# Kernel tuning notes

Hardware: AMD Instinct MI355X
Metric: run time of the kernel (lower is better)

## Reference

```python
import jax, jax.numpy as jnp
import numpy as np

B, C, H, W = 128, 512, 14, 14
WIN, SHIFT = 7, 3
HEADS, HD = 16, 32
HID = 2048
EPS = 1e-5
N = WIN * WIN
NWH = H // WIN
NW = NWH * NWH


def _rel_pos_index():
    coords = np.stack(np.meshgrid(np.arange(WIN), np.arange(WIN), indexing='ij'))  # (2,Wh,Ww)
    flat = coords.reshape(2, -1)
    rel = (flat[:, :, None] - flat[:, None, :]).transpose(1, 2, 0)  # (N,N,2)
    rel[..., 0] += WIN - 1
    rel[..., 1] += WIN - 1
    rel[..., 0] *= 2 * WIN - 1
    return rel.sum(-1)  # (N,N) in [0, (2W-1)^2)


def _attn_mask():
    img = np.zeros((H, W))
    cnt = 0
    for h in (slice(0, -WIN), slice(-WIN, -SHIFT), slice(-SHIFT, None)):
        for w in (slice(0, -WIN), slice(-WIN, -SHIFT), slice(-SHIFT, None)):
            img[h, w] = cnt
            cnt += 1
    mw = img.reshape(NWH, WIN, NWH, WIN).transpose(0, 2, 1, 3).reshape(-1, N)  # (nW,N)
    d = mw[:, None, :] - mw[:, :, None]
    return np.where(d != 0, -100.0, 0.0).astype(np.float32)  # (nW,N,N)


REL_IDX = _rel_pos_index()
ATTN_MASK = jnp.asarray(_attn_mask())


def _ln_c(x, w, b):
    # LayerNorm2d: normalize over channel dim of NCHW
    mu = x.mean(axis=1, keepdims=True)
    var = ((x - mu) ** 2).mean(axis=1, keepdims=True)
    xn = (x - mu) * jax.lax.rsqrt(var + EPS)
    return xn * w[None, :, None, None] + b[None, :, None, None]


def setup_inputs() -> dict:
    key = jax.random.key(0)
    ks = jax.random.split(key, 12)
    s = 0.02
    return {
        'x': jax.random.normal(ks[0], (B, C, H, W), jnp.float32),
        'ln1_w': jnp.ones((C,), jnp.float32),
        'ln1_b': jnp.zeros((C,), jnp.float32),
        'qkv_w': jax.random.normal(ks[1], (3 * C, C), jnp.float32) * s,
        'qkv_b': jnp.zeros((3 * C,), jnp.float32),
        'rel_bias': jax.random.normal(ks[2], ((2 * WIN - 1) ** 2, HEADS), jnp.float32) * s,
        'proj_w': jax.random.normal(ks[3], (C, C), jnp.float32) * s,
        'proj_b': jnp.zeros((C,), jnp.float32),
        'gamma1': jnp.full((C,), 1e-6, jnp.float32),
        'ln2_w': jnp.ones((C,), jnp.float32),
        'ln2_b': jnp.zeros((C,), jnp.float32),
        'fc1_w': jax.random.normal(ks[4], (HID, C), jnp.float32) * s,
        'fc1_b': jnp.zeros((HID,), jnp.float32),
        'fc2_w': jax.random.normal(ks[5], (C, HID), jnp.float32) * s,
        'fc2_b': jnp.zeros((C,), jnp.float32),
        'gamma2': jnp.full((C,), 1e-6, jnp.float32),
    }


def reference(x, ln1_w, ln1_b, qkv_w, qkv_b, rel_bias, proj_w, proj_b, gamma1,
              ln2_w, ln2_b, fc1_w, fc1_b, fc2_w, fc2_b, gamma2):
    # ---- shifted-window attention branch ----
    y = _ln_c(x, ln1_w, ln1_b).transpose(0, 2, 3, 1)  # (B,H,W,C)
    y = jnp.roll(y, (-SHIFT, -SHIFT), axis=(1, 2))
    # window partition -> (B*nW, N, C)
    xw = y.reshape(B, NWH, WIN, NWH, WIN, C).transpose(0, 1, 3, 2, 4, 5).reshape(B * NW, N, C)
    qkv = (xw @ qkv_w.T + qkv_b).reshape(B * NW, N, 3, HEADS, HD).transpose(2, 0, 3, 1, 4)
    q, k, v = qkv[0], qkv[1], qkv[2]  # (B*nW, heads, N, hd)
    attn = jnp.einsum('bhnd,bhmd->bhnm', q * (HD ** -0.5), k)
    bias = rel_bias[REL_IDX.reshape(-1)].reshape(N, N, HEADS).transpose(2, 0, 1)  # (heads,N,N)
    attn = attn + bias[None]
    attn = attn.reshape(B, NW, HEADS, N, N) + ATTN_MASK[None, :, None]
    attn = jax.nn.softmax(attn.reshape(B * NW, HEADS, N, N), axis=-1)
    out = jnp.einsum('bhnm,bhmd->bhnd', attn, v).transpose(0, 2, 1, 3).reshape(B * NW, N, C)
    out = out @ proj_w.T + proj_b
    # window reverse + roll back
    y = out.reshape(B, NWH, NWH, WIN, WIN, C).transpose(0, 1, 3, 2, 4, 5).reshape(B, H, W, C)
    y = jnp.roll(y, (SHIFT, SHIFT), axis=(1, 2))
    y = gamma1 * y  # layer scale over channel (last dim in NHWC)
    x = x + y.transpose(0, 3, 1, 2)
    # ---- MLP branch ----
    z = _ln_c(x, ln2_w, ln2_b).transpose(0, 2, 3, 1)  # (B,H,W,C)
    z = jax.nn.gelu(z @ fc1_w.T + fc1_b, approximate=False)
    z = z @ fc2_w.T + fc2_b
    z = gamma2 * z
    return x + z.transpose(0, 3, 1, 2)
```

## Files before the change

kernel.cpp:

```cpp
#include <hip/hip_runtime.h>
#include <cmath>
#include <cstdint>

typedef float floatx4 __attribute__((ext_vector_type(4)));

#define EPS_ 1e-5f
#define QSCALE 0.17677669529663689f

__device__ __forceinline__ void gload16(const uint8_t* g, uint8_t* l) {
  __builtin_amdgcn_global_load_lds(
      (const __attribute__((address_space(1))) void*)g,
      (__attribute__((address_space(3))) void*)l, 16, 0, 0);
}

template<bool HI>
__device__ __forceinline__ int pk_fp8(float a, float b, int old) {
  return __builtin_amdgcn_cvt_pk_fp8_f32(a, b, old, HI);
}
__device__ __forceinline__ int pk_fp8x4(float v0, float v1, float v2, float v3) {
  int w = pk_fp8<false>(v0, v1, 0);
  return pk_fp8<true>(v2, v3, w);
}

__device__ __forceinline__ uint16_t f2bf(float f) {
  uint32_t u = __float_as_uint(f);
  return (uint16_t)((u + 0x7fffu + ((u >> 16) & 1u)) >> 16);
}
__device__ __forceinline__ float bf2f(uint16_t h) {
  return __uint_as_float(((uint32_t)h) << 16);
}

__device__ __forceinline__ float fast_gelu(float v) {
  const float t = __expf(-1.702f * v);
  return v * __builtin_amdgcn_rcpf(1.f + t);
}


template<int K>
__global__ void cvt_frag(const float* __restrict__ s, uint8_t* __restrict__ d, int n4) {
  const int i = blockIdx.x * 256 + threadIdx.x;
  if (i >= n4) return;
  const int kq = K >> 2;
  const int n = i / kq;
  const int k = (i - n * kq) << 2;
  const float4 v = ((const float4*)s)[i];
  const int panel = ((n >> 6) << 2) + (n & 3);
  const int lm = (n >> 2) & 15;
  const long addr = (long)panel * (16 * K) + ((k >> 3) << 7) + (lm << 3) + (k & 4);
  *(int*)(d + addr) = pk_fp8x4(v.x, v.y, v.z, v.w);
}

__global__ __launch_bounds__(256)
void ln_stats_nchw(const float* __restrict__ x, float* __restrict__ mu, float* __restrict__ rs) {
  const int tl = threadIdx.x & 63;
  const int wv = threadIdx.x >> 6;
  const int t = blockIdx.x * 64 + tl;
  const int b = t / 196;
  const int p = t - b * 196;
  const float* xp = x + (long)b * 100352 + p;
  float s = 0.f, ss = 0.f;
  const int cbeg = wv * 128;
  for (int c = cbeg; c < cbeg + 128; ++c) {
    const float v = xp[(long)c * 196];
    s += v; ss += v * v;
  }
  __shared__ float sb[4][64], qb[4][64];
  sb[wv][tl] = s; qb[wv][tl] = ss;
  __syncthreads();
  if (wv == 0) {
    s  = sb[0][tl] + sb[1][tl] + sb[2][tl] + sb[3][tl];
    ss = qb[0][tl] + qb[1][tl] + qb[2][tl] + qb[3][tl];
    const float m = s * (1.f / 512.f);
    const float var = ss * (1.f / 512.f) - m * m;
    mu[t] = m;
    rs[t] = rsqrtf(var + EPS_);
  }
}

__global__ __launch_bounds__(256)
void ln1_apply(const float* __restrict__ x, const float* __restrict__ mu, const float* __restrict__ rs,
               const float* __restrict__ w, const float* __restrict__ bb, uint8_t* __restrict__ A) {
  __shared__ float tile[64][53];
  const int bid = blockIdx.x;
  const int ct = bid & 7;
  const int pt = (bid >> 3) & 3;
  const int b = bid >> 5;
  const int p0 = pt * 49, c0 = ct * 64;
  const long xbase = (long)b * 100352;
  for (int idx = threadIdx.x; idx < 3136; idx += 256) {
    const int cl = idx / 49;
    const int pl = idx - cl * 49;
    tile[cl][pl] = x[xbase + (long)(c0 + cl) * 196 + p0 + pl];
  }
  __syncthreads();
  const int tbase = b * 196 + p0;
  for (int idx = threadIdx.x; idx < 784; idx += 256) {
    const int pl = idx >> 4;
    const int cq = (idx & 15) << 2;
    const int t = tbase + pl;
    const int c = c0 + cq;
    const float m = mu[t], rr = rs[t];
    const float v0 = (tile[cq + 0][pl] - m) * rr * w[c + 0] + bb[c + 0];
    const float v1 = (tile[cq + 1][pl] - m) * rr * w[c + 1] + bb[c + 1];
    const float v2 = (tile[cq + 2][pl] - m) * rr * w[c + 2] + bb[c + 2];
    const float v3 = (tile[cq + 3][pl] - m) * rr * w[c + 3] + bb[c + 3];
    const long addr = (long)(t & ~15) * 512 + ((c >> 3) << 7) + ((t & 15) << 3) + (c & 4);
    *(int*)(A + addr) = pk_fp8x4(v0, v1, v2, v3);
  }
}

__global__ __launch_bounds__(256)
void ln2_panel(const uint16_t* __restrict__ Xb, const float* __restrict__ S1,
               const float* __restrict__ S2, const float* __restrict__ w,
               const float* __restrict__ bb, uint8_t* __restrict__ Z) {
  __shared__ float xs[16 * 516];
  const int p = blockIdx.x;
  const int t0 = p * 16;
  for (int idx = threadIdx.x; idx < 1024; idx += 256) {
    const int tl = idx >> 6;
    const int c8 = (idx & 63) << 3;
    const uint4 raw = *(const uint4*)(Xb + ((long)(t0 + tl) << 9) + c8);
    float* xr = xs + tl * 516 + c8;
    xr[0] = bf2f((uint16_t)(raw.x & 0xffff)); xr[1] = bf2f((uint16_t)(raw.x >> 16));
    xr[2] = bf2f((uint16_t)(raw.y & 0xffff)); xr[3] = bf2f((uint16_t)(raw.y >> 16));
    xr[4] = bf2f((uint16_t)(raw.z & 0xffff)); xr[5] = bf2f((uint16_t)(raw.z >> 16));
    xr[6] = bf2f((uint16_t)(raw.w & 0xffff)); xr[7] = bf2f((uint16_t)(raw.w >> 16));
  }
  __syncthreads();
  uint8_t* zp = Z + (long)p * 8192;
  for (int e = threadIdx.x; e < 2048; e += 256) {
    const int off = e << 2;
    const int k8 = off >> 7;
    const int tl = (off >> 3) & 15;
    const int c = (k8 << 3) + (off & 4);
    const int t = t0 + tl;
    const float m = S1[t] * (1.f / 512.f);
    const float var = S2[t] * (1.f / 512.f) - m * m;
    const float r = rsqrtf(var + EPS_);
    const float* xr = xs + tl * 516 + c;
    const float v0 = (xr[0] - m) * r * w[c + 0] + bb[c + 0];
    const float v1 = (xr[1] - m) * r * w[c + 1] + bb[c + 1];
    const float v2 = (xr[2] - m) * r * w[c + 2] + bb[c + 2];
    const float v3 = (xr[3] - m) * r * w[c + 3] + bb[c + 3];
    *(int*)(zp + off) = pk_fp8x4(v0, v1, v2, v3);
  }
}

template<int MI, int K, int EPI, int NG, int T>
__global__ __launch_bounds__(256, 4)
void gemm_bl(const uint8_t* __restrict__ A, const uint8_t* __restrict__ Bw,
             const float* __restrict__ bias, const float* __restrict__ res,
             const uint16_t* __restrict__ resb, const float* __restrict__ gamma,
             uint8_t* __restrict__ outb, float* __restrict__ outf,
             uint16_t* __restrict__ outh, float* __restrict__ S1, float* __restrict__ S2,
             const int N) {
  const int kx = blockIdx.x & 7;
  const int sx = blockIdx.x >> 3;
  const int t = (sx / NG) * 8 + kx;
  if (t >= T) return;
  const int g = sx - (sx / NG) * NG;
  __shared__ __align__(16) uint8_t Bs[(EPI == 3) ? 33280 : 32768];
  const int tid = threadIdx.x;
  const int wave = tid >> 6, lane = tid & 63;
  const int lm = lane & 15, lq = lane >> 4;
  const long m0 = (long)t * (MI * 64);
  const long n0 = (long)g << 6;
  const uint8_t* abase = A + (m0 + wave * MI * 16) * (long)K + (lane << 3);
  floatx4 acc[MI][4] = {};
  constexpr int NKS = K / 32;
  long aP0[MI], aP1[MI];
  #pragma unroll
  for (int i = 0; i < MI; ++i) {
    aP0[i] = *(const long*)(abase + (long)i * 16 * K);
    aP1[i] = *(const long*)(abase + (long)i * 16 * K + 512);
  }
  #pragma unroll
  for (int ph = 0; ph < K / 512; ++ph) {
    const uint8_t* bsrc = Bw + n0 * K + ph * 8192;
    #pragma unroll
    for (int j = 0; j < 4; ++j)
      #pragma unroll
      for (int c = 0; c < 2; ++c)
        gload16(bsrc + (long)j * 16 * K + c * 4096 + tid * 16,
                Bs + j * 8192 + c * 4096 + tid * 16);
    __syncthreads();
    #pragma unroll
    for (int ksl = 0; ksl < 16; ++ksl) {
      const int sg = ph * 16 + ksl;
      long aC[MI];
      #pragma unroll
      for (int i = 0; i < MI; ++i) aC[i] = (ksl & 1) ? aP1[i] : aP0[i];
      if (sg + 2 < NKS) {
        #pragma unroll
        for (int i = 0; i < MI; ++i) {
          const long v = *(const long*)(abase + (long)i * 16 * K + (long)(sg + 2) * 512);
          if (ksl & 1) aP1[i] = v; else aP0[i] = v;
        }
      }
      long bf[4];
      #pragma unroll
      for (int j = 0; j < 4; ++j)
        bf[j] = *(const long*)(Bs + j * 8192 + ksl * 512 + (lane << 3));
      __builtin_amdgcn_s_setprio(1);
      #pragma unroll
      for (int i = 0; i < MI; ++i)
        #pragma unroll
        for (int j = 0; j < 4; ++j)
          acc[i][j] = __builtin_amdgcn_mfma_f32_16x16x32_fp8_fp8(aC[i], bf[j], acc[i][j], 0, 0, 0);
      __builtin_amdgcn_s_setprio(0);
    }
    if (K / 512 > 1 && ph + 1 < K / 512) __syncthreads();
  }
  const int cb = (g << 6) + (lm << 2);
  const float4 b4 = *(const float4*)(bias + cb);
  float4 g4 = make_float4(0.f, 0.f, 0.f, 0.f);
  if (EPI == 1 || EPI == 3) g4 = *(const float4*)(gamma + cb);
  const float qs = (EPI == 0 && cb < 512) ? QSCALE : 1.f;
  if (EPI != 3) {
    #pragma unroll
    for (int i = 0; i < MI; ++i) {
      #pragma unroll
      for (int r = 0; r < 4; ++r) {
        const long rowg = m0 + wave * MI * 16 + i * 16 + lq * 4 + r;
        float v0 = acc[i][0][r] + b4.x;
        float v1 = acc[i][1][r] + b4.y;
        float v2 = acc[i][2][r] + b4.z;
        float v3 = acc[i][3][r] + b4.w;
        if (EPI == 0) {
          *(int*)(outb + rowg * (long)N + cb) = pk_fp8x4(v0 * qs, v1 * qs, v2 * qs, v3 * qs);
        } else if (EPI == 2) {
          v0 = fast_gelu(v0);
          v1 = fast_gelu(v1);
          v2 = fast_gelu(v2);
          v3 = fast_gelu(v3);
          const long addr = (rowg & ~15L) * 2048 + ((cb >> 3) << 7) + ((rowg & 15) << 3) + (cb & 4);
          *(int*)(outb + addr) = pk_fp8x4(v0, v1, v2, v3);
        } else {
          const unsigned rg = (unsigned)rowg;
          const unsigned bi = rg / 196u;
          const unsigned p = rg - bi * 196u;
          const float* xr = res + (long)bi * 100352 + p;
          const float o0 = xr[(long)(cb + 0) * 196] + g4.x * v0;
          const float o1 = xr[(long)(cb + 1) * 196] + g4.y * v1;
          const float o2 = xr[(long)(cb + 2) * 196] + g4.z * v2;
          const float o3 = xr[(long)(cb + 3) * 196] + g4.w * v3;
          ushort4 hv;
          hv.x = f2bf(o0); hv.y = f2bf(o1); hv.z = f2bf(o2); hv.w = f2bf(o3);
          *(ushort4*)(outh + rowg * 512 + cb) = hv;
          const float q0 = bf2f(hv.x), q1 = bf2f(hv.y), q2 = bf2f(hv.z), q3 = bf2f(hv.w);
          float s = q0 + q1 + q2 + q3;
          float ss = q0 * q0 + q1 * q1 + q2 * q2 + q3 * q3;
          s += __shfl_xor(s, 1);  ss += __shfl_xor(ss, 1);
          s += __shfl_xor(s, 2);  ss += __shfl_xor(ss, 2);
          s += __shfl_xor(s, 4);  ss += __shfl_xor(ss, 4);
          s += __shfl_xor(s, 8);  ss += __shfl_xor(ss, 8);
          if (lm == 0) {
            atomicAdd(S1 + rowg, s);
            atomicAdd(S2 + rowg, ss);
          }
        }
      }
    }
  } else {
    float* Tx = (float*)Bs;
    __syncthreads();
    #pragma unroll
    for (int i = 0; i < MI; ++i) {
      #pragma unroll
      for (int r = 0; r < 4; ++r) {
        const long rowg = m0 + wave * MI * 16 + i * 16 + lq * 4 + r;
        const int rl = (int)(rowg - m0);
        const ushort4 rb = *(const ushort4*)(resb + rowg * 512 + cb);
        Tx[(lm * 4 + 0) * 129 + rl] = bf2f(rb.x) + g4.x * (acc[i][0][r] + b4.x);
        Tx[(lm * 4 + 1) * 129 + rl] = bf2f(rb.y) + g4.y * (acc[i][1][r] + b4.y);
        Tx[(lm * 4 + 2) * 129 + rl] = bf2f(rb.z) + g4.z * (acc[i][2][r] + b4.z);
        Tx[(lm * 4 + 3) * 129 + rl] = bf2f(rb.w) + g4.w * (acc[i][3][r] + b4.w);
      }
    }
    __syncthreads();
    #pragma unroll
    for (int t2 = 0; t2 < 32; ++t2) {
      const int idx = t2 * 256 + tid;
      const int rl = idx & 127;
      const int ch = idx >> 7;
      const unsigned m = (unsigned)(m0 + rl);
      const unsigned bi = m / 196u;
      const unsigned p = m - bi * 196u;
      outf[(long)bi * 100352 + (long)(n0 + ch) * 196 + p] = Tx[ch * 129 + rl];
    }
  }
}

__global__ __launch_bounds__(256)
void bm_build(const float* __restrict__ rel_bias, float* __restrict__ BM) {
  const int hw = blockIdx.x;
  const int head = hw >> 2, wpos = hw & 3;
  const int wi = wpos >> 1, wj = wpos & 1;
  for (int k = 0; k < 4; ++k) {
    const int idx = k * 256 + threadIdx.x;
    const int tile = idx >> 6, l = idx & 63;
    const int qi = tile >> 2, ti = tile & 3;
    const int n = l & 15, g = l >> 4;
    const int query = qi * 16 + n;
    const int qy = query / 7, qx = query - qy * 7;
    const int hh = wi * 7 + qy, ww = wj * 7 + qx;
    const int ri = (hh < 7 ? 0 : (hh < 11 ? 1 : 2)) * 3 + (ww < 7 ? 0 : (ww < 11 ? 1 : 2));
    float4 ov;
    float vv[4];
    #pragma unroll
    for (int r = 0; r < 4; ++r) {
      const int key = ti * 16 + g * 4 + r;
      float v;
      if (query >= 49 || key >= 49) {
        v = -3.0e38f;
      } else {
        const int ky = key / 7, kx = key - ky * 7;
        const int bidx = (qy - ky + 6) * 13 + (qx - kx + 6);
        const int h2 = wi * 7 + ky, w2 = wj * 7 + kx;
        const int rj = (h2 < 7 ? 0 : (h2 < 11 ? 1 : 2)) * 3 + (w2 < 7 ? 0 : (w2 < 11 ? 1 : 2));
        v = rel_bias[bidx * 16 + head] + ((ri != rj) ? -100.f : 0.f);
      }
      vv[r] = v;
    }
    ov.x = vv[0]; ov.y = vv[1]; ov.z = vv[2]; ov.w = vv[3];
    *(float4*)(BM + ((long)(hw * 16 + tile) << 8) + l * 4) = ov;
  }
}

__device__ __forceinline__ void tr4(const uint32_t d[4], uint32_t o[4]) {
  #pragma unroll
  for (int c = 0; c < 4; ++c)
    o[c] = ((d[0] >> (8 * c)) & 0xffu) | (((d[1] >> (8 * c)) & 0xffu) << 8)
         | (((d[2] >> (8 * c)) & 0xffu) << 16) | (((d[3] >> (8 * c)) & 0xffu) << 24);
}

__global__ __launch_bounds__(256)
void attn_mfma(const uint8_t* __restrict__ QKV, const float* __restrict__ BM,
               uint8_t* __restrict__ AT) {
  __shared__ uint8_t lds[4][9984];
  const int wave = threadIdx.x >> 6, lane = threadIdx.x & 63;
  const int n = lane & 15, g = lane >> 4;
  const int gw = blockIdx.x * 4 + wave;
  const int wd = gw >> 4, head = gw & 15;
  const int b = wd >> 2, wpos = wd & 3;
  const int wi = wpos >> 1, wj = wpos & 1;
  uint8_t* Pb = lds[wave];
  uint8_t* Vt = lds[wave] + 4608;
  uint8_t* Ot = lds[wave] + 6912;
  const long base = (long)b * 196 * 1536;
  auto tok = [&](int slot) -> int {
    const int ty = slot / 7, tx = slot - ty * 7;
    int h = wi * 7 + ty + 3; if (h >= 14) h -= 14;
    int w = wj * 7 + tx + 3; if (w >= 14) w -= 14;
    return h * 14 + w;
  };
  long Ak[4], Bq[4];
  #pragma unroll
  for (int t4 = 0; t4 < 4; ++t4) {
    int slot = t4 * 16 + n; if (slot > 48) slot = 48;
    const long tb = base + (long)tok(slot) * 1536 + head * 32 + g * 8;
    Bq[t4] = *(const long*)(QKV + tb);
    Ak[t4] = *(const long*)(QKV + tb + 512);
  }
  #pragma unroll
  for (int bb2 = 0; bb2 < 2; ++bb2) {
    const int blk = lane + bb2 * 64;
    const int dq = blk >> 4, tq = blk & 15;
    uint32_t d4[4], o4[4];
    #pragma unroll
    for (int r = 0; r < 4; ++r) {
      int slot = tq * 4 + r; if (slot > 48) slot = 48;
      d4[r] = *(const uint32_t*)(QKV + base + (long)tok(slot) * 1536 + 1024 + head * 32 + dq * 4);
    }
    tr4(d4, o4);
    #pragma unroll
    for (int c = 0; c < 4; ++c)
      *(uint32_t*)(Vt + (dq * 4 + c) * 72 + tq * 4) = o4[c];
  }
  floatx4 acc[4][4];
  const float* bmw = BM + ((long)(head * 4 + wpos) << 12) + lane * 4;
  #pragma unroll
  for (int qi = 0; qi < 4; ++qi)
    #pragma unroll
    for (int ti = 0; ti < 4; ++ti) {
      const float4 bv = *(const float4*)(bmw + ((qi * 4 + ti) << 8));
      acc[qi][ti][0] = bv.x; acc[qi][ti][1] = bv.y;
      acc[qi][ti][2] = bv.z; acc[qi][ti][3] = bv.w;
    }
  #pragma unroll
  for (int qi = 0; qi < 4; ++qi)
    #pragma unroll
    for (int ti = 0; ti < 4; ++ti)
      acc[qi][ti] = __builtin_amdgcn_mfma_f32_16x16x32_fp8_fp8(Ak[ti], Bq[qi], acc[qi][ti], 0, 0, 0);
  #pragma unroll
  for (int qi = 0; qi < 4; ++qi) {
    float mx = -3.0e38f;
    #pragma unroll
    for (int ti = 0; ti < 4; ++ti)
      #pragma unroll
      for (int r = 0; r < 4; ++r) mx = fmaxf(mx, acc[qi][ti][r]);
    mx = fmaxf(mx, __shfl_xor(mx, 16));
    mx = fmaxf(mx, __shfl_xor(mx, 32));
    float sum = 0.f;
    #pragma unroll
    for (int ti = 0; ti < 4; ++ti)
      #pragma unroll
      for (int r = 0; r < 4; ++r) {
        const float e = __expf(acc[qi][ti][r] - mx);
        acc[qi][ti][r] = e; sum += e;
      }
    sum += __shfl_xor(sum, 16);
    sum += __shfl_xor(sum, 32);
    const float inv = 1.f / sum;
    #pragma unroll
    for (int ti = 0; ti < 4; ++ti) {
      const int pw = pk_fp8x4(acc[qi][ti][0] * inv, acc[qi][ti][1] * inv,
                              acc[qi][ti][2] * inv, acc[qi][ti][3] * inv);
      *(uint32_t*)(Pb + (qi * 16 + n) * 72 + ti * 16 + g * 4) = pw;
    }
  }
  asm volatile("s_waitcnt lgkmcnt(0)" ::: "memory");
  long Bv[2][2];
  #pragma unroll
  for (int ni = 0; ni < 2; ++ni)
    #pragma unroll
    for (int s = 0; s < 2; ++s)
      Bv[ni][s] = *(const long*)(Vt + (ni * 16 + n) * 72 + s * 32 + g * 8);
  floatx4 o[4][2] = {};
  #pragma unroll
  for (int qi = 0; qi < 4; ++qi)
    #pragma unroll
    for (int s = 0; s < 2; ++s) {
      const long Ap = *(const long*)(Pb + (qi * 16 + n) * 72 + s * 32 + g * 8);
      #pragma unroll
      for (int ni = 0; ni < 2; ++ni)
        o[qi][ni] = __builtin_amdgcn_mfma_f32_16x16x32_fp8_fp8(Ap, Bv[ni][s], o[qi][ni], 0, 0, 0);
    }
  #pragma unroll
  for (int qi = 0; qi < 4; ++qi)
    #pragma unroll
    for (int ni = 0; ni < 2; ++ni)
      #pragma unroll
      for (int r = 0; r < 4; ++r)
        Ot[(qi * 16 + g * 4 + r) * 48 + ni * 16 + n] =
            (uint8_t)(pk_fp8<false>(o[qi][ni][r], 0.f, 0) & 0xff);
  asm volatile("s_waitcnt lgkmcnt(0)" ::: "memory");
  if (lane < 49) {
    const int m = b * 196 + tok(lane);
    uint8_t* opb = AT + (long)(m & ~15) * 512 + ((m & 15) << 3);
    #pragma unroll
    for (int d8 = 0; d8 < 4; ++d8)
      *(long*)(opb + (head * 4 + d8) * 128) = *(const long*)(Ot + lane * 48 + d8 * 8);
  }
}

extern "C" void kernel_launch(void* const* d_in, const int* in_sizes, int n_in,
                              void* d_out, int out_size, void* d_ws, size_t ws_size,
                              hipStream_t stream) {
  const float* x      = (const float*)d_in[0];
  const float* ln1_w  = (const float*)d_in[1];
  const float* ln1_b  = (const float*)d_in[2];
  const float* qkv_w  = (const float*)d_in[3];
  const float* qkv_b  = (const float*)d_in[4];
  const float* relb   = (const float*)d_in[5];
  const float* proj_w = (const float*)d_in[6];
  const float* proj_b = (const float*)d_in[7];
  const float* gamma1 = (const float*)d_in[8];
  const float* ln2_w  = (const float*)d_in[9];
  const float* ln2_b  = (const float*)d_in[10];
  const float* fc1_w  = (const float*)d_in[11];
  const float* fc1_b  = (const float*)d_in[12];
  const float* fc2_w  = (const float*)d_in[13];
  const float* fc2_b  = (const float*)d_in[14];
  const float* gamma2 = (const float*)d_in[15];
  float* out = (float*)d_out;
  char* ws = (char*)d_ws;

  float*    mu1 = (float*)(ws + 0);
  float*    rs1 = (float*)(ws + 100352);
  float*    S1  = (float*)(ws + 200704);
  float*    S2  = (float*)(ws + 301056);
  uint8_t*  Wq  = (uint8_t*)(ws + 401408);
  uint8_t*  Wp  = (uint8_t*)(ws + 1187840);
  uint8_t*  W1  = (uint8_t*)(ws + 1449984);
  uint8_t*  W2  = (uint8_t*)(ws + 2498560);
  float*    BMt = (float*)  (ws + 3547136);
  uint8_t*  Afp = (uint8_t*)(ws + 4595712);
  uint16_t* X1b = (uint16_t*)(ws + 68820992);
  uint8_t*  QKV = (uint8_t*)(ws + 120201216);
  uint8_t*  AT  = (uint8_t*)(ws + 158736384);
  uint8_t*  Hb  = (uint8_t*)(ws + 120201216);

  hipMemsetAsync(ws + 200704, 0, 200704, stream);

  cvt_frag<512> <<<768,  256, 0, stream>>>(qkv_w, Wq, 196608);
  cvt_frag<512> <<<256,  256, 0, stream>>>(proj_w, Wp, 65536);
  cvt_frag<512> <<<1024, 256, 0, stream>>>(fc1_w, W1, 262144);
  cvt_frag<2048><<<1024, 256, 0, stream>>>(fc2_w, W2, 262144);
  bm_build<<<64, 256, 0, stream>>>(relb, BMt);

  ln_stats_nchw<<<392, 256, 0, stream>>>(x, mu1, rs1);
  ln1_apply<<<4096, 256, 0, stream>>>(x, mu1, rs1, ln1_w, ln1_b, Afp);

  gemm_bl<4, 512, 0, 24, 98><<<2496, 256, 0, stream>>>(Afp, Wq, qkv_b, nullptr, nullptr, nullptr, QKV, nullptr, nullptr, nullptr, nullptr, 1536);

  attn_mfma<<<2048, 256, 0, stream>>>(QKV, BMt, AT);

  gemm_bl<4, 512, 1, 8, 98><<<832, 256, 0, stream>>>(AT, Wp, proj_b, x, nullptr, gamma1, nullptr, nullptr, X1b, S1, S2, 512);

  ln2_panel<<<1568, 256, 0, stream>>>(X1b, S1, S2, ln2_w, ln2_b, Afp);

  gemm_bl<4, 512, 2, 32, 98><<<3328, 256, 0, stream>>>(Afp, W1, fc1_b, nullptr, nullptr, nullptr, Hb, nullptr, nullptr, nullptr, nullptr, 2048);
  gemm_bl<2, 2048, 3, 8, 196><<<1600, 256, 0, stream>>>(Hb, W2, fc2_b, nullptr, X1b, gamma2, nullptr, out, nullptr, nullptr, nullptr, 512);
}
```

Before: 388.1 us.

## Use MX-scaled 32x32x64 FP8 MFMA for fc1 GEMM with new operand layouts

Replaces the fc1 GEMM with a dedicated kernel using the gfx950 scaled 32x32x64 f8f6f4 MFMA (unit scales), which does more work per instruction than the previous FP8 MFMA path. The LN2 output layout and the fc1 weight conversion are changed to match the new operand fragment layouts, and the GELU epilogue writes FP8 pairs into the existing layout that fc2 expects. A operands are read straight from global memory rather than staged through shared memory, and the output stores narrow to 2-byte writes, which may hurt memory efficiency.

```diff
diff --git a/kernel.cpp b/kernel.cpp
--- a/kernel.cpp
+++ b/kernel.cpp
@@ -3,6 +3,9 @@
 #include <cstdint>
 
 typedef float floatx4 __attribute__((ext_vector_type(4)));
+typedef float floatx16 __attribute__((ext_vector_type(16)));
+typedef int   intx4   __attribute__((ext_vector_type(4)));
+typedef int   intx8   __attribute__((ext_vector_type(8)));
 
 #define EPS_ 1e-5f
 #define QSCALE 0.17677669529663689f
@@ -33,6 +36,14 @@
 __device__ __forceinline__ float fast_gelu(float v) {
   const float t = __expf(-1.702f * v);
   return v * __builtin_amdgcn_rcpf(1.f + t);
+}
+
+__device__ __forceinline__ intx8 cat8(intx4 a, intx4 b) {
+  return __builtin_shufflevector(a, b, 0, 1, 2, 3, 4, 5, 6, 7);
+}
+__device__ __forceinline__ floatx16 mfma_mx(intx8 a, intx8 b, floatx16 c) {
+  return __builtin_amdgcn_mfma_scale_f32_32x32x64_f8f6f4(
+      a, b, c, 0, 0, 0, 0x7F7F7F7F, 0, 0x7F7F7F7F);
 }
 
 
@@ -47,6 +58,18 @@
   const int panel = ((n >> 6) << 2) + (n & 3);
   const int lm = (n >> 2) & 15;
   const long addr = (long)panel * (16 * K) + ((k >> 3) << 7) + (lm << 3) + (k & 4);
+  *(int*)(d + addr) = pk_fp8x4(v.x, v.y, v.z, v.w);
+}
+
+__global__ void cvt_frag_mx512(const float* __restrict__ s, uint8_t* __restrict__ d, int n4) {
+  const int i = blockIdx.x * 256 + threadIdx.x;
+  if (i >= n4) return;
+  const int n = i >> 7;
+  const int k = (i & 127) << 2;
+  const float4 v = ((const float4*)s)[i];
+  const long addr = (long)(n >> 6) * 32768 + (n & 1) * 16384 + ((k >> 6) << 11)
+                  + (((k >> 4) & 1) << 10)
+                  + ((((k >> 5) & 1) << 5) + ((n & 63) >> 1)) * 16 + (k & 15);
   *(int*)(d + addr) = pk_fp8x4(v.x, v.y, v.z, v.w);
 }
 
@@ -127,12 +150,9 @@
     xr[6] = bf2f((uint16_t)(raw.w & 0xffff)); xr[7] = bf2f((uint16_t)(raw.w >> 16));
   }
   __syncthreads();
-  uint8_t* zp = Z + (long)p * 8192;
   for (int e = threadIdx.x; e < 2048; e += 256) {
-    const int off = e << 2;
-    const int k8 = off >> 7;
-    const int tl = (off >> 3) & 15;
-    const int c = (k8 << 3) + (off & 4);
+    const int tl = e >> 7;
+    const int c  = (e & 127) << 2;
     const int t = t0 + tl;
     const float m = S1[t] * (1.f / 512.f);
     const float var = S2[t] * (1.f / 512.f) - m * m;
@@ -142,7 +162,8 @@
     const float v1 = (xr[1] - m) * r * w[c + 1] + bb[c + 1];
     const float v2 = (xr[2] - m) * r * w[c + 2] + bb[c + 2];
     const float v3 = (xr[3] - m) * r * w[c + 3] + bb[c + 3];
-    *(int*)(zp + off) = pk_fp8x4(v0, v1, v2, v3);
+    const long addr = (long)(t >> 5) * 16384 + ((c >> 5) << 10) + ((t & 31) << 5) + (c & 31);
+    *(int*)(Z + addr) = pk_fp8x4(v0, v1, v2, v3);
   }
 }
 
@@ -228,13 +249,6 @@
         float v3 = acc[i][3][r] + b4.w;
         if (EPI == 0) {
           *(int*)(outb + rowg * (long)N + cb) = pk_fp8x4(v0 * qs, v1 * qs, v2 * qs, v3 * qs);
-        } else if (EPI == 2) {
-          v0 = fast_gelu(v0);
-          v1 = fast_gelu(v1);
-          v2 = fast_gelu(v2);
-          v3 = fast_gelu(v3);
-          const long addr = (rowg & ~15L) * 2048 + ((cb >> 3) << 7) + ((rowg & 15) << 3) + (cb & 4);
-          *(int*)(outb + addr) = pk_fp8x4(v0, v1, v2, v3);
         } else {
           const unsigned rg = (unsigned)rowg;
           const unsigned bi = rg / 196u;
@@ -291,6 +305,59 @@
   }
 }
 
+__global__ __launch_bounds__(256, 4)
+void gemm_mx_fc1(const uint8_t* __restrict__ A, const uint8_t* __restrict__ Bw,
+                 const float* __restrict__ bias, uint8_t* __restrict__ outb) {
+  const int kx = blockIdx.x & 7;
+  const int sx = blockIdx.x >> 3;
+  const int t = (sx >> 5) * 8 + kx;
+  if (t >= 98) return;
+  const int g = sx & 31;
+  __shared__ __align__(16) uint8_t Bs[32768];
+  const int tid = threadIdx.x;
+  const int wave = tid >> 6, lane = tid & 63;
+  const long m0 = (long)t * 256;
+  const int n0 = g << 6;
+  const uint8_t* bsrc = Bw + (long)n0 * 512;
+  #pragma unroll
+  for (int c = 0; c < 8; ++c)
+    gload16(bsrc + c * 4096 + tid * 16, Bs + c * 4096 + tid * 16);
+  const uint8_t* ab0 = A + (m0 + wave * 64) * 512 + lane * 32;
+  const uint8_t* ab1 = ab0 + 16384;
+  floatx16 acc[2][2] = {};
+  __syncthreads();
+  #pragma unroll
+  for (int s = 0; s < 8; ++s) {
+    const intx8 a0 = cat8(*(const intx4*)(ab0 + s * 2048), *(const intx4*)(ab0 + s * 2048 + 16));
+    const intx8 a1 = cat8(*(const intx4*)(ab1 + s * 2048), *(const intx4*)(ab1 + s * 2048 + 16));
+    const intx8 b0 = cat8(*(const intx4*)(Bs + s * 2048 + lane * 16),
+                          *(const intx4*)(Bs + s * 2048 + 1024 + lane * 16));
+    const intx8 b1 = cat8(*(const intx4*)(Bs + 16384 + s * 2048 + lane * 16),
+                          *(const intx4*)(Bs + 16384 + s * 2048 + 1024 + lane * 16));
+    acc[0][0] = mfma_mx(a0, b0, acc[0][0]);
+    acc[0][1] = mfma_mx(a0, b1, acc[0][1]);
+    acc[1][0] = mfma_mx(a1, b0, acc[1][0]);
+    acc[1][1] = mfma_mx(a1, b1, acc[1][1]);
+  }
+  const int cp = lane & 31;
+  const int c0 = n0 + 2 * cp;
+  const float2 b2 = *(const float2*)(bias + c0);
+  const int rbase = (int)m0 + wave * 64 + 4 * (lane >> 5);
+  #pragma unroll
+  for (int ri = 0; ri < 2; ++ri)
+    #pragma unroll
+    for (int q = 0; q < 16; ++q) {
+      const int row = rbase + ri * 32 + (q & 3) + 8 * (q >> 2);
+      float v0 = acc[ri][0][q] + b2.x;
+      float v1 = acc[ri][1][q] + b2.y;
+      v0 = fast_gelu(v0);
+      v1 = fast_gelu(v1);
+      const int w = pk_fp8<false>(v0, v1, 0);
+      const long addr = (long)(row & ~15) * 2048 + ((c0 >> 3) << 7) + ((row & 15) << 3) + (c0 & 7);
+      *(uint16_t*)(outb + addr) = (uint16_t)(w & 0xffff);
+    }
+}
+
 __global__ __launch_bounds__(256)
 void bm_build(const float* __restrict__ rel_bias, float* __restrict__ BM) {
   const int hw = blockIdx.x;
@@ -495,7 +562,7 @@
 
   cvt_frag<512> <<<768,  256, 0, stream>>>(qkv_w, Wq, 196608);
   cvt_frag<512> <<<256,  256, 0, stream>>>(proj_w, Wp, 65536);
-  cvt_frag<512> <<<1024, 256, 0, stream>>>(fc1_w, W1, 262144);
+  cvt_frag_mx512<<<1024, 256, 0, stream>>>(fc1_w, W1, 262144);
   cvt_frag<2048><<<1024, 256, 0, stream>>>(fc2_w, W2, 262144);
   bm_build<<<64, 256, 0, stream>>>(relb, BMt);
 
@@ -510,6 +577,7 @@
 
   ln2_panel<<<1568, 256, 0, stream>>>(X1b, S1, S2, ln2_w, ln2_b, Afp);
 
-  gemm_bl<4, 512, 2, 32, 98><<<3328, 256, 0, stream>>>(Afp, W1, fc1_b, nullptr, nullptr, nullptr, Hb, nullptr, nullptr, nullptr, nullptr, 2048);
+  gemm_mx_fc1<<<3328, 256, 0, stream>>>(Afp, W1, fc1_b, Hb);
+
   gemm_bl<2, 2048, 3, 8, 196><<<1600, 256, 0, stream>>>(Hb, W2, fc2_b, nullptr, X1b, gamma2, nullptr, out, nullptr, nullptr, nullptr, 512);
 }
```

After: 385.5 us. Within noise of the previous version (-0.7%).
